# Optimization experiments

Hardware: AMD Instinct MI355X
Metric: run time of the kernel (lower is better)

## Reference

```python
import jax, jax.numpy as jnp
import numpy as np

SIZES = [384, 160, 128, 96, 1]   # aev_length followed by hidden sizes (ANI-1 config)
N_SPECIES = 4                    # H, C, N, O
N_LAYERS = 4
CELU_ALPHA = 0.1
B, A = 128, 512                  # molecules, atoms per molecule


def setup_inputs() -> dict:
    key = jax.random.key(0)
    ks = jax.random.split(key, 2 + 2 * N_LAYERS)
    inp = {
        "fullaev": jax.random.normal(ks[0], (B, A, SIZES[0]), dtype=jnp.float32),
        "species": jax.random.randint(ks[1], (A,), 0, N_SPECIES, dtype=jnp.int32),
    }
    # Per-species stacked Linear params, torch default init: U(-1/sqrt(fan_in), 1/sqrt(fan_in))
    for l in range(N_LAYERS):
        bound = 1.0 / np.sqrt(SIZES[l])
        inp[f"W{l}"] = jax.random.uniform(ks[2 + 2 * l], (N_SPECIES, SIZES[l + 1], SIZES[l]),
                                          dtype=jnp.float32, minval=-bound, maxval=bound)
        inp[f"b{l}"] = jax.random.uniform(ks[3 + 2 * l], (N_SPECIES, SIZES[l + 1]),
                                          dtype=jnp.float32, minval=-bound, maxval=bound)
    return inp


def reference(fullaev, species, W0, b0, W1, b1, W2, b2, W3, b3):
    # fullaev: [B, A, aev_len]; species: [A] int route ids.
    # Equivalent to the per-atom Python loop: each atom goes through its
    # species' MLP; gather the per-atom weight matrices and do one batched GEMM per layer.
    Ws = (W0, W1, W2, W3)
    bs = (b0, b1, b2, b3)
    y = fullaev
    for l in range(N_LAYERS):
        Wa = Ws[l][species]          # [A, out, in] gathered per atom
        ba = bs[l][species]          # [A, out]
        y = jnp.einsum('bai,aoi->bao', y, Wa) + ba[None, :, :]
        if l < N_LAYERS - 1:
            y = jax.nn.celu(y, alpha=CELU_ALPHA)
    # stack over atoms + sum reducer over atom dim, then squeeze -> [B]
    return jnp.squeeze(jnp.sum(y, axis=1), axis=-1)
```

## Files before the change

### kernel.cpp

```cpp
#include <hip/hip_runtime.h>


typedef float f32x4 __attribute__((ext_vector_type(4)));
typedef short s16x8 __attribute__((ext_vector_type(8)));

#define NMOL   128
#define NATOM  512
#define AEV    384
#define XLD    136
#define Y0LD   168
#define Y1LD   136
#define Y2LD   104

#define PL0    61440
#define PL1    20480
#define PL2    12288
#define BASE0  0
#define BASE1  245760
#define BASE2  327680
#define WP_BYTE_OFF 262144

__device__ __forceinline__ ushort f2bf(float f) {
    uint u = __float_as_uint(f);
    return (ushort)((u + 0x7fffu + ((u >> 16) & 1u)) >> 16);
}
__device__ __forceinline__ float bf2f(ushort h) {
    return __uint_as_float(((uint)h) << 16);
}
__device__ __forceinline__ float celu_f(float v) {
    return fmaxf(v, 0.0f) + fminf(0.1f * (__expf(10.0f * v) - 1.0f), 0.0f);
}

__global__ __launch_bounds__(256) void prep_kernel(
    const float* __restrict__ W0, const float* __restrict__ W1,
    const float* __restrict__ W2, ushort* __restrict__ Wp)
{
    const int idx = blockIdx.x * 256 + threadIdx.x;
    int n, k0, KS;
    size_t base;
    const float* src;
    if (idx < 30720) {
        const int s = idx / 7680, r = idx % 7680;
        n = r / 48; k0 = (r % 48) * 8; KS = 12;
        src = W0 + (size_t)idx * 8;
        base = BASE0 + (size_t)s * PL0;
    } else if (idx < 40960) {
        const int i2 = idx - 30720;
        const int s = i2 / 2560, r = i2 % 2560;
        n = r / 20; k0 = (r % 20) * 8; KS = 5;
        src = W1 + (size_t)i2 * 8;
        base = BASE1 + (size_t)s * PL1;
    } else {
        const int i2 = idx - 40960;
        const int s = i2 / 1536, r = i2 % 1536;
        n = r / 16; k0 = (r % 16) * 8; KS = 4;
        src = W2 + (size_t)i2 * 8;
        base = BASE2 + (size_t)s * PL2;
    }
    const float4 v0 = *(const float4*)(src);
    const float4 v1 = *(const float4*)(src + 4);
    const size_t fo = (size_t)((((n >> 4) * KS + (k0 >> 5)) * 64
                                + ((k0 & 31) >> 3) * 16 + (n & 15)) * 8);
    uint4 w;
    w.x = (uint)f2bf(v0.x) | ((uint)f2bf(v0.y) << 16);
    w.y = (uint)f2bf(v0.z) | ((uint)f2bf(v0.w) << 16);
    w.z = (uint)f2bf(v1.x) | ((uint)f2bf(v1.y) << 16);
    w.w = (uint)f2bf(v1.z) | ((uint)f2bf(v1.w) << 16);
    *(uint4*)(Wp + base + fo) = w;
}

__global__ __launch_bounds__(512, 4) void ani_mfma_kernel(
    const float* __restrict__ aev, const int* __restrict__ species,
    const ushort* __restrict__ Wp,
    const float* __restrict__ b0, const float* __restrict__ b1,
    const float* __restrict__ b2,
    const float* __restrict__ W3, const float* __restrict__ b3,
    float* __restrict__ partial)
{
    __shared__ __align__(16) ushort xbuf[NMOL * XLD];
    __shared__ __align__(16) ushort ybuf[NMOL * Y0LD];

    const int a    = blockIdx.x;
    const int tid  = threadIdx.x;
    const int lane = tid & 63;
    const int wid  = tid >> 6;
    const int mgrp = wid >> 2;
    const int ngrp = wid & 3;
    const bool has3 = (ngrp < 2);

    const int mol0 = tid >> 5;
    const int c4   = tid & 31;
    const size_t PSTR = (size_t)16 * NATOM * AEV;
    const float* xp = aev + ((size_t)mol0 * NATOM + a) * AEV + c4 * 4;

    const int s = species[a];
    const ushort* Bh0 = Wp + BASE0 + (size_t)s * PL0;
    const ushort* Bh1 = Wp + BASE1 + (size_t)s * PL1;
    const ushort* Bh2 = Wp + BASE2 + (size_t)s * PL2;
    const float* b0s = b0 + s * 160;
    const float* b1s = b1 + s * 128;
    const float* b2s = b2 + s * 96;
    const float* w3s = W3 + s * 96;
    const float  bb3 = b3[s];

    float4 rv[8];
    auto prefetch_rv = [&](int t) {
        #pragma unroll
        for (int p = 0; p < 8; ++p)
            rv[p] = *(const float4*)(xp + t * 128 + p * PSTR);
    };
    auto stage = [&]() {
        #pragma unroll
        for (int p = 0; p < 8; ++p) {
            uint2 ph;
            ph.x = (uint)f2bf(rv[p].x) | ((uint)f2bf(rv[p].y) << 16);
            ph.y = (uint)f2bf(rv[p].z) | ((uint)f2bf(rv[p].w) << 16);
            *(uint2*)(xbuf + (mol0 + 16 * p) * XLD + c4 * 4) = ph;
        }
    };

    f32x4 acc[4][3];
    const f32x4 zero = {0.f, 0.f, 0.f, 0.f};
    #pragma unroll
    for (int mf = 0; mf < 4; ++mf)
        #pragma unroll
        for (int t = 0; t < 3; ++t) acc[mf][t] = zero;

    prefetch_rv(0);
    stage();
    __syncthreads();

    #pragma unroll
    for (int tile = 0; tile < 3; ++tile) {
        if (tile < 2) prefetch_rv(tile + 1);
        #pragma unroll
        for (int ks = 0; ks < 4; ++ks) {
            const int gks = tile * 4 + ks;
            const s16x8 bh0 = *(const s16x8*)(Bh0 + ((size_t)((ngrp    ) * 12 + gks) * 64 + lane) * 8);
            const s16x8 bh1 = *(const s16x8*)(Bh0 + ((size_t)((ngrp + 4) * 12 + gks) * 64 + lane) * 8);
            s16x8 bh2;
            if (has3) bh2 = *(const s16x8*)(Bh0 + ((size_t)((ngrp + 8) * 12 + gks) * 64 + lane) * 8);
            s16x8 ah[4];
            #pragma unroll
            for (int mf = 0; mf < 4; ++mf)
                ah[mf] = *(const s16x8*)(xbuf + (mgrp * 64 + mf * 16 + (lane & 15)) * XLD
                                         + ks * 32 + (lane >> 4) * 8);
            #pragma unroll
            for (int mf = 0; mf < 4; ++mf) {
                acc[mf][0] = __builtin_amdgcn_mfma_f32_16x16x32_bf16(ah[mf], bh0, acc[mf][0], 0, 0, 0);
                acc[mf][1] = __builtin_amdgcn_mfma_f32_16x16x32_bf16(ah[mf], bh1, acc[mf][1], 0, 0, 0);
            }
            if (has3) {
                #pragma unroll
                for (int mf = 0; mf < 4; ++mf)
                    acc[mf][2] = __builtin_amdgcn_mfma_f32_16x16x32_bf16(ah[mf], bh2, acc[mf][2], 0, 0, 0);
            }
        }
        __syncthreads();
        if (tile < 2) {
            stage();
            __syncthreads();
        }
    }

    s16x8 b1r[2][5];
    #pragma unroll
    for (int ks = 0; ks < 5; ++ks) {
        b1r[0][ks] = *(const s16x8*)(Bh1 + ((size_t)((ngrp    ) * 5 + ks) * 64 + lane) * 8);
        b1r[1][ks] = *(const s16x8*)(Bh1 + ((size_t)((ngrp + 4) * 5 + ks) * 64 + lane) * 8);
    }

    #pragma unroll
    for (int t = 0; t < 3; ++t) {
        if (t < 2 || has3) {
            const int n = (ngrp + 4 * t) * 16 + (lane & 15);
            const float bv = b0s[n];
            #pragma unroll
            for (int mf = 0; mf < 4; ++mf) {
                #pragma unroll
                for (int r = 0; r < 4; ++r) {
                    const int row = mgrp * 64 + mf * 16 + (lane >> 4) * 4 + r;
                    ybuf[row * Y0LD + n] = f2bf(celu_f(acc[mf][t][r] + bv));
                }
            }
        }
    }
    __syncthreads();

    f32x4 acc1[4][2];
    #pragma unroll
    for (int mf = 0; mf < 4; ++mf) { acc1[mf][0] = zero; acc1[mf][1] = zero; }
    #pragma unroll
    for (int ks = 0; ks < 5; ++ks) {
        s16x8 ah[4];
        #pragma unroll
        for (int mf = 0; mf < 4; ++mf)
            ah[mf] = *(const s16x8*)(ybuf + (mgrp * 64 + mf * 16 + (lane & 15)) * Y0LD
                                     + ks * 32 + (lane >> 4) * 8);
        #pragma unroll
        for (int mf = 0; mf < 4; ++mf) {
            acc1[mf][0] = __builtin_amdgcn_mfma_f32_16x16x32_bf16(ah[mf], b1r[0][ks], acc1[mf][0], 0, 0, 0);
            acc1[mf][1] = __builtin_amdgcn_mfma_f32_16x16x32_bf16(ah[mf], b1r[1][ks], acc1[mf][1], 0, 0, 0);
        }
    }

    s16x8 b2r[2][4];
    #pragma unroll
    for (int ks = 0; ks < 4; ++ks)
        b2r[0][ks] = *(const s16x8*)(Bh2 + ((size_t)((ngrp) * 4 + ks) * 64 + lane) * 8);
    if (has3) {
        #pragma unroll
        for (int ks = 0; ks < 4; ++ks)
            b2r[1][ks] = *(const s16x8*)(Bh2 + ((size_t)((ngrp + 4) * 4 + ks) * 64 + lane) * 8);
    }

    #pragma unroll
    for (int t = 0; t < 2; ++t) {
        const int n = (ngrp + 4 * t) * 16 + (lane & 15);
        const float bv = b1s[n];
        #pragma unroll
        for (int mf = 0; mf < 4; ++mf) {
            #pragma unroll
            for (int r = 0; r < 4; ++r) {
                const int row = mgrp * 64 + mf * 16 + (lane >> 4) * 4 + r;
                xbuf[row * Y1LD + n] = f2bf(celu_f(acc1[mf][t][r] + bv));
            }
        }
    }
    __syncthreads();

    f32x4 acc2[4][2];
    #pragma unroll
    for (int mf = 0; mf < 4; ++mf) { acc2[mf][0] = zero; acc2[mf][1] = zero; }
    #pragma unroll
    for (int ks = 0; ks < 4; ++ks) {
        s16x8 ah[4];
        #pragma unroll
        for (int mf = 0; mf < 4; ++mf)
            ah[mf] = *(const s16x8*)(xbuf + (mgrp * 64 + mf * 16 + (lane & 15)) * Y1LD
                                     + ks * 32 + (lane >> 4) * 8);
        #pragma unroll
        for (int mf = 0; mf < 4; ++mf) {
            acc2[mf][0] = __builtin_amdgcn_mfma_f32_16x16x32_bf16(ah[mf], b2r[0][ks], acc2[mf][0], 0, 0, 0);
            if (has3)
                acc2[mf][1] = __builtin_amdgcn_mfma_f32_16x16x32_bf16(ah[mf], b2r[1][ks], acc2[mf][1], 0, 0, 0);
        }
    }
    __syncthreads();

    #pragma unroll
    for (int t = 0; t < 2; ++t) {
        if (t == 0 || has3) {
            const int n = (ngrp + 4 * t) * 16 + (lane & 15);
            const float bv = b2s[n];
            #pragma unroll
            for (int mf = 0; mf < 4; ++mf) {
                #pragma unroll
                for (int r = 0; r < 4; ++r) {
                    const int row = mgrp * 64 + mf * 16 + (lane >> 4) * 4 + r;
                    ybuf[row * Y2LD + n] = f2bf(celu_f(acc2[mf][t][r] + bv));
                }
            }
        }
    }
    __syncthreads();

    {
        float* red = (float*)xbuf;
        const int m = tid & (NMOL - 1);
        const int q = tid >> 7;
        float accv = 0.f;
        #pragma unroll
        for (int ii = 0; ii < 24; ++ii) {
            const int i = q * 24 + ii;
            accv = fmaf(w3s[i], bf2f(ybuf[m * Y2LD + i]), accv);
        }
        red[q * NMOL + m] = accv;
        __syncthreads();
        if (tid < NMOL) {
            const float sm = red[tid] + red[NMOL + tid] + red[2 * NMOL + tid]
                           + red[3 * NMOL + tid] + bb3;
            partial[(size_t)a * NMOL + tid] = sm;
        }
    }
}

__global__ __launch_bounds__(256) void reduce_kernel(
    const float* __restrict__ partial, float* __restrict__ out)
{
    __shared__ float red[256];
    const int m = blockIdx.x;
    const int t = threadIdx.x;
    float sv = partial[(size_t)t * NMOL + m] + partial[(size_t)(t + 256) * NMOL + m];
    red[t] = sv;
    __syncthreads();
    #pragma unroll
    for (int w = 128; w > 0; w >>= 1) {
        if (t < w) red[t] += red[t + w];
        __syncthreads();
    }
    if (t == 0) out[m] = red[0];
}

extern "C" void kernel_launch(void* const* d_in, const int* in_sizes, int n_in,
                              void* d_out, int out_size, void* d_ws, size_t ws_size,
                              hipStream_t stream) {
    const float* aev     = (const float*)d_in[0];
    const int*   species = (const int*)  d_in[1];
    const float* W0 = (const float*)d_in[2];
    const float* b0 = (const float*)d_in[3];
    const float* W1 = (const float*)d_in[4];
    const float* b1 = (const float*)d_in[5];
    const float* W2 = (const float*)d_in[6];
    const float* b2 = (const float*)d_in[7];
    const float* W3 = (const float*)d_in[8];
    const float* b3 = (const float*)d_in[9];
    float* out     = (float*)d_out;
    float* partial = (float*)d_ws;
    ushort* Wp     = (ushort*)((char*)d_ws + WP_BYTE_OFF);

    prep_kernel<<<184, 256, 0, stream>>>(W0, W1, W2, Wp);
    ani_mfma_kernel<<<NATOM, 512, 0, stream>>>(aev, species, Wp,
                                               b0, b1, b2, W3, b3, partial);
    reduce_kernel<<<NMOL, 256, 0, stream>>>(partial, out);
}
```

Baseline: 44.57 us.

## Double-buffer layer-0 input staging in LDS with smaller K tiles

Splits the layer-0 input staging into six K=64 tiles held in two LDS buffers, with a two-slot register prefetch that runs two tiles ahead. Each tile now needs one barrier instead of two, so the next tile can be staged while the current one is being multiplied. This trades fewer MFMA steps per barrier and slightly more LDS for less barrier stall on the global loads. The launch-bounds attribute is restated in explicit amdgpu attribute form.

```diff
diff --git a/kernel.cpp b/kernel.cpp
--- a/kernel.cpp
+++ b/kernel.cpp
@@ -7,7 +7,7 @@
 #define NMOL   128
 #define NATOM  512
 #define AEV    384
-#define XLD    136
+#define XLD    72
 #define Y0LD   168
 #define Y1LD   136
 #define Y2LD   104
@@ -69,7 +69,9 @@
     *(uint4*)(Wp + base + fo) = w;
 }
 
-__global__ __launch_bounds__(512, 4) void ani_mfma_kernel(
+__global__ __attribute__((amdgpu_flat_work_group_size(512, 512),
+                          amdgpu_waves_per_eu(4, 4)))
+void ani_mfma_kernel(
     const float* __restrict__ aev, const int* __restrict__ species,
     const ushort* __restrict__ Wp,
     const float* __restrict__ b0, const float* __restrict__ b1,
@@ -77,7 +79,7 @@
     const float* __restrict__ W3, const float* __restrict__ b3,
     float* __restrict__ partial)
 {
-    __shared__ __align__(16) ushort xbuf[NMOL * XLD];
+    __shared__ __align__(16) ushort xbuf[2 * NMOL * XLD];
     __shared__ __align__(16) ushort ybuf[NMOL * Y0LD];
 
     const int a    = blockIdx.x;
@@ -88,9 +90,9 @@
     const int ngrp = wid & 3;
     const bool has3 = (ngrp < 2);
 
-    const int mol0 = tid >> 5;
-    const int c4   = tid & 31;
-    const size_t PSTR = (size_t)16 * NATOM * AEV;
+    const int mol0 = tid >> 4;
+    const int c4   = tid & 15;
+    const size_t PSTR = (size_t)32 * NATOM * AEV;
     const float* xp = aev + ((size_t)mol0 * NATOM + a) * AEV + c4 * 4;
 
     const int s = species[a];
@@ -103,19 +105,22 @@
     const float* w3s = W3 + s * 96;
     const float  bb3 = b3[s];
 
-    float4 rv[8];
-    auto prefetch_rv = [&](int t) {
-        #pragma unroll
-        for (int p = 0; p < 8; ++p)
-            rv[p] = *(const float4*)(xp + t * 128 + p * PSTR);
+    ushort* X0 = xbuf;
+    ushort* X1 = xbuf + NMOL * XLD;
+
+    float4 rv[2][4];
+    auto prefetch_rv = [&](int slot, int t) {
+        #pragma unroll
+        for (int p = 0; p < 4; ++p)
+            rv[slot][p] = *(const float4*)(xp + t * 64 + p * PSTR);
     };
-    auto stage = [&]() {
-        #pragma unroll
-        for (int p = 0; p < 8; ++p) {
+    auto stage = [&](ushort* dst, int slot) {
+        #pragma unroll
+        for (int p = 0; p < 4; ++p) {
             uint2 ph;
-            ph.x = (uint)f2bf(rv[p].x) | ((uint)f2bf(rv[p].y) << 16);
-            ph.y = (uint)f2bf(rv[p].z) | ((uint)f2bf(rv[p].w) << 16);
-            *(uint2*)(xbuf + (mol0 + 16 * p) * XLD + c4 * 4) = ph;
+            ph.x = (uint)f2bf(rv[slot][p].x) | ((uint)f2bf(rv[slot][p].y) << 16);
+            ph.y = (uint)f2bf(rv[slot][p].z) | ((uint)f2bf(rv[slot][p].w) << 16);
+            *(uint2*)(dst + (mol0 + 32 * p) * XLD + c4 * 4) = ph;
         }
     };
 
@@ -126,16 +131,20 @@
         #pragma unroll
         for (int t = 0; t < 3; ++t) acc[mf][t] = zero;
 
-    prefetch_rv(0);
-    stage();
-    __syncthreads();
-
-    #pragma unroll
-    for (int tile = 0; tile < 3; ++tile) {
-        if (tile < 2) prefetch_rv(tile + 1);
-        #pragma unroll
-        for (int ks = 0; ks < 4; ++ks) {
-            const int gks = tile * 4 + ks;
+    prefetch_rv(0, 0);
+    stage(X0, 0);
+    prefetch_rv(1, 1);
+    __syncthreads();
+
+    #pragma unroll
+    for (int t = 0; t < 6; ++t) {
+        const int cur = t & 1;
+        ushort* Xc = cur ? X1 : X0;
+        ushort* Xn = cur ? X0 : X1;
+        if (t < 4) prefetch_rv(cur, t + 2);
+        #pragma unroll
+        for (int ks = 0; ks < 2; ++ks) {
+            const int gks = t * 2 + ks;
             const s16x8 bh0 = *(const s16x8*)(Bh0 + ((size_t)((ngrp    ) * 12 + gks) * 64 + lane) * 8);
             const s16x8 bh1 = *(const s16x8*)(Bh0 + ((size_t)((ngrp + 4) * 12 + gks) * 64 + lane) * 8);
             s16x8 bh2;
@@ -143,7 +152,7 @@
             s16x8 ah[4];
             #pragma unroll
             for (int mf = 0; mf < 4; ++mf)
-                ah[mf] = *(const s16x8*)(xbuf + (mgrp * 64 + mf * 16 + (lane & 15)) * XLD
+                ah[mf] = *(const s16x8*)(Xc + (mgrp * 64 + mf * 16 + (lane & 15)) * XLD
                                          + ks * 32 + (lane >> 4) * 8);
             #pragma unroll
             for (int mf = 0; mf < 4; ++mf) {
@@ -156,9 +165,8 @@
                     acc[mf][2] = __builtin_amdgcn_mfma_f32_16x16x32_bf16(ah[mf], bh2, acc[mf][2], 0, 0, 0);
             }
         }
-        __syncthreads();
-        if (tile < 2) {
-            stage();
+        if (t < 5) {
+            stage(Xn, cur ^ 1);
             __syncthreads();
         }
     }
```

Result: faster. 42.97 us (-3.6%).

## Load layer-0 A fragments directly from global, drop LDS staging of AEV

Applied to the files above, without the earlier changes.

Layer 0 no longer stages the AEV tile through shared memory with syncs between K tiles. Each wave now loads its MFMA A-fragments straight from global memory, converts them to bf16 in registers, and works on a different wave tiling (4 M-groups by 2 N-groups, 5 N-fragments each). This is meant to remove the LDS round trip and barriers from the dominant GEMM. In exchange the global loads are strided per lane, there is no explicit prefetch, and register pressure rises with 10 accumulators. The launch-bounds attribute is also switched to explicit waves-per-eu.

```diff
diff --git a/kernel.cpp b/kernel.cpp
--- a/kernel.cpp
+++ b/kernel.cpp
@@ -1,4 +1,5 @@
 #include <hip/hip_runtime.h>
+#include <hip/hip_bf16.h>
 
 
 typedef float f32x4 __attribute__((ext_vector_type(4)));
@@ -7,7 +8,6 @@
 #define NMOL   128
 #define NATOM  512
 #define AEV    384
-#define XLD    136
 #define Y0LD   168
 #define Y1LD   136
 #define Y2LD   104
@@ -29,6 +29,12 @@
 }
 __device__ __forceinline__ float celu_f(float v) {
     return fmaxf(v, 0.0f) + fminf(0.1f * (__expf(10.0f * v) - 1.0f), 0.0f);
+}
+__device__ __forceinline__ uint pk2bf(float x, float y) {
+    __hip_bfloat162 h2;
+    h2.x = __float2bfloat16(x);
+    h2.y = __float2bfloat16(y);
+    return *(uint*)&h2;
 }
 
 __global__ __launch_bounds__(256) void prep_kernel(
@@ -69,7 +75,9 @@
     *(uint4*)(Wp + base + fo) = w;
 }
 
-__global__ __launch_bounds__(512, 4) void ani_mfma_kernel(
+__global__ __attribute__((amdgpu_flat_work_group_size(512, 512),
+                          amdgpu_waves_per_eu(4, 4)))
+void ani_mfma_kernel(
     const float* __restrict__ aev, const int* __restrict__ species,
     const ushort* __restrict__ Wp,
     const float* __restrict__ b0, const float* __restrict__ b1,
@@ -77,21 +85,13 @@
     const float* __restrict__ W3, const float* __restrict__ b3,
     float* __restrict__ partial)
 {
-    __shared__ __align__(16) ushort xbuf[NMOL * XLD];
-    __shared__ __align__(16) ushort ybuf[NMOL * Y0LD];
+    __shared__ __align__(16) ushort y0buf[NMOL * Y0LD];
+    __shared__ __align__(16) ushort y1buf[NMOL * Y1LD];
 
     const int a    = blockIdx.x;
     const int tid  = threadIdx.x;
     const int lane = tid & 63;
     const int wid  = tid >> 6;
-    const int mgrp = wid >> 2;
-    const int ngrp = wid & 3;
-    const bool has3 = (ngrp < 2);
-
-    const int mol0 = tid >> 5;
-    const int c4   = tid & 31;
-    const size_t PSTR = (size_t)16 * NATOM * AEV;
-    const float* xp = aev + ((size_t)mol0 * NATOM + a) * AEV + c4 * 4;
 
     const int s = species[a];
     const ushort* Bh0 = Wp + BASE0 + (size_t)s * PL0;
@@ -103,177 +103,158 @@
     const float* w3s = W3 + s * 96;
     const float  bb3 = b3[s];
 
-    float4 rv[8];
-    auto prefetch_rv = [&](int t) {
-        #pragma unroll
-        for (int p = 0; p < 8; ++p)
-            rv[p] = *(const float4*)(xp + t * 128 + p * PSTR);
-    };
-    auto stage = [&]() {
-        #pragma unroll
-        for (int p = 0; p < 8; ++p) {
-            uint2 ph;
-            ph.x = (uint)f2bf(rv[p].x) | ((uint)f2bf(rv[p].y) << 16);
-            ph.y = (uint)f2bf(rv[p].z) | ((uint)f2bf(rv[p].w) << 16);
-            *(uint2*)(xbuf + (mol0 + 16 * p) * XLD + c4 * 4) = ph;
-        }
-    };
-
-    f32x4 acc[4][3];
     const f32x4 zero = {0.f, 0.f, 0.f, 0.f};
-    #pragma unroll
-    for (int mf = 0; mf < 4; ++mf)
-        #pragma unroll
-        for (int t = 0; t < 3; ++t) acc[mf][t] = zero;
-
-    prefetch_rv(0);
-    stage();
-    __syncthreads();
-
-    #pragma unroll
-    for (int tile = 0; tile < 3; ++tile) {
-        if (tile < 2) prefetch_rv(tile + 1);
-        #pragma unroll
-        for (int ks = 0; ks < 4; ++ks) {
-            const int gks = tile * 4 + ks;
-            const s16x8 bh0 = *(const s16x8*)(Bh0 + ((size_t)((ngrp    ) * 12 + gks) * 64 + lane) * 8);
-            const s16x8 bh1 = *(const s16x8*)(Bh0 + ((size_t)((ngrp + 4) * 12 + gks) * 64 + lane) * 8);
-            s16x8 bh2;
-            if (has3) bh2 = *(const s16x8*)(Bh0 + ((size_t)((ngrp + 8) * 12 + gks) * 64 + lane) * 8);
-            s16x8 ah[4];
-            #pragma unroll
-            for (int mf = 0; mf < 4; ++mf)
-                ah[mf] = *(const s16x8*)(xbuf + (mgrp * 64 + mf * 16 + (lane & 15)) * XLD
-                                         + ks * 32 + (lane >> 4) * 8);
-            #pragma unroll
-            for (int mf = 0; mf < 4; ++mf) {
-                acc[mf][0] = __builtin_amdgcn_mfma_f32_16x16x32_bf16(ah[mf], bh0, acc[mf][0], 0, 0, 0);
-                acc[mf][1] = __builtin_amdgcn_mfma_f32_16x16x32_bf16(ah[mf], bh1, acc[mf][1], 0, 0, 0);
-            }
-            if (has3) {
+
+    {
+        const int mgrp0 = wid >> 1;
+        const int ngrp0 = wid & 1;
+        const float* arow = aev + ((size_t)(mgrp0 * 32 + (lane & 15)) * NATOM + a) * AEV
+                            + (lane >> 4) * 8;
+        const size_t AMF = (size_t)16 * NATOM * AEV;
+
+        f32x4 acc0[2][5];
+        #pragma unroll
+        for (int mf = 0; mf < 2; ++mf)
+            #pragma unroll
+            for (int nf = 0; nf < 5; ++nf) acc0[mf][nf] = zero;
+
+        #pragma unroll
+        for (int gks = 0; gks < 12; ++gks) {
+            s16x8 ah[2];
+            #pragma unroll
+            for (int mf = 0; mf < 2; ++mf) {
+                const float* ap = arow + mf * AMF + gks * 32;
+                const float4 lo = *(const float4*)(ap);
+                const float4 hi = *(const float4*)(ap + 4);
+                union { s16x8 v; uint u[4]; } r;
+                r.u[0] = pk2bf(lo.x, lo.y);
+                r.u[1] = pk2bf(lo.z, lo.w);
+                r.u[2] = pk2bf(hi.x, hi.y);
+                r.u[3] = pk2bf(hi.z, hi.w);
+                ah[mf] = r.v;
+            }
+            #pragma unroll
+            for (int nf = 0; nf < 5; ++nf) {
+                const s16x8 bh = *(const s16x8*)(
+                    Bh0 + ((size_t)((ngrp0 * 5 + nf) * 12 + gks) * 64 + lane) * 8);
+                acc0[0][nf] = __builtin_amdgcn_mfma_f32_16x16x32_bf16(ah[0], bh, acc0[0][nf], 0, 0, 0);
+                acc0[1][nf] = __builtin_amdgcn_mfma_f32_16x16x32_bf16(ah[1], bh, acc0[1][nf], 0, 0, 0);
+            }
+        }
+
+        #pragma unroll
+        for (int nf = 0; nf < 5; ++nf) {
+            const int n = (ngrp0 * 5 + nf) * 16 + (lane & 15);
+            const float bv = b0s[n];
+            #pragma unroll
+            for (int mf = 0; mf < 2; ++mf) {
                 #pragma unroll
-                for (int mf = 0; mf < 4; ++mf)
-                    acc[mf][2] = __builtin_amdgcn_mfma_f32_16x16x32_bf16(ah[mf], bh2, acc[mf][2], 0, 0, 0);
-            }
-        }
-        __syncthreads();
-        if (tile < 2) {
-            stage();
-            __syncthreads();
-        }
-    }
-
+                for (int r = 0; r < 4; ++r) {
+                    const int row = mgrp0 * 32 + mf * 16 + (lane >> 4) * 4 + r;
+                    y0buf[row * Y0LD + n] = f2bf(celu_f(acc0[mf][nf][r] + bv));
+                }
+            }
+        }
+    }
+
+    const int mgrp = wid >> 2;
+    const int ngrp = wid & 3;
+    const bool has3 = (ngrp < 2);
     s16x8 b1r[2][5];
     #pragma unroll
     for (int ks = 0; ks < 5; ++ks) {
         b1r[0][ks] = *(const s16x8*)(Bh1 + ((size_t)((ngrp    ) * 5 + ks) * 64 + lane) * 8);
         b1r[1][ks] = *(const s16x8*)(Bh1 + ((size_t)((ngrp + 4) * 5 + ks) * 64 + lane) * 8);
     }
-
-    #pragma unroll
-    for (int t = 0; t < 3; ++t) {
-        if (t < 2 || has3) {
+    __syncthreads();
+
+    f32x4 acc1[4][2];
+    #pragma unroll
+    for (int mf = 0; mf < 4; ++mf) { acc1[mf][0] = zero; acc1[mf][1] = zero; }
+    #pragma unroll
+    for (int ks = 0; ks < 5; ++ks) {
+        s16x8 ah[4];
+        #pragma unroll
+        for (int mf = 0; mf < 4; ++mf)
+            ah[mf] = *(const s16x8*)(y0buf + (mgrp * 64 + mf * 16 + (lane & 15)) * Y0LD
+                                     + ks * 32 + (lane >> 4) * 8);
+        #pragma unroll
+        for (int mf = 0; mf < 4; ++mf) {
+            acc1[mf][0] = __builtin_amdgcn_mfma_f32_16x16x32_bf16(ah[mf], b1r[0][ks], acc1[mf][0], 0, 0, 0);
+            acc1[mf][1] = __builtin_amdgcn_mfma_f32_16x16x32_bf16(ah[mf], b1r[1][ks], acc1[mf][1], 0, 0, 0);
+        }
+    }
+
+    s16x8 b2r[2][4];
+    #pragma unroll
+    for (int ks = 0; ks < 4; ++ks)
+        b2r[0][ks] = *(const s16x8*)(Bh2 + ((size_t)((ngrp) * 4 + ks) * 64 + lane) * 8);
+    if (has3) {
+        #pragma unroll
+        for (int ks = 0; ks < 4; ++ks)
+            b2r[1][ks] = *(const s16x8*)(Bh2 + ((size_t)((ngrp + 4) * 4 + ks) * 64 + lane) * 8);
+    }
+
+    #pragma unroll
+    for (int t = 0; t < 2; ++t) {
+        const int n = (ngrp + 4 * t) * 16 + (lane & 15);
+        const float bv = b1s[n];
+        #pragma unroll
+        for (int mf = 0; mf < 4; ++mf) {
+            #pragma unroll
+            for (int r = 0; r < 4; ++r) {
+                const int row = mgrp * 64 + mf * 16 + (lane >> 4) * 4 + r;
+                y1buf[row * Y1LD + n] = f2bf(celu_f(acc1[mf][t][r] + bv));
+            }
+        }
+    }
+    __syncthreads();
+
+    f32x4 acc2[4][2];
+    #pragma unroll
+    for (int mf = 0; mf < 4; ++mf) { acc2[mf][0] = zero; acc2[mf][1] = zero; }
+    #pragma unroll
+    for (int ks = 0; ks < 4; ++ks) {
+        s16x8 ah[4];
+        #pragma unroll
+        for (int mf = 0; mf < 4; ++mf)
+            ah[mf] = *(const s16x8*)(y1buf + (mgrp * 64 + mf * 16 + (lane & 15)) * Y1LD
+                                     + ks * 32 + (lane >> 4) * 8);
+        #pragma unroll
+        for (int mf = 0; mf < 4; ++mf) {
+            acc2[mf][0] = __builtin_amdgcn_mfma_f32_16x16x32_bf16(ah[mf], b2r[0][ks], acc2[mf][0], 0, 0, 0);
+            if (has3)
+                acc2[mf][1] = __builtin_amdgcn_mfma_f32_16x16x32_bf16(ah[mf], b2r[1][ks], acc2[mf][1], 0, 0, 0);
+        }
+    }
+    __syncthreads();
+
+    #pragma unroll
+    for (int t = 0; t < 2; ++t) {
+        if (t == 0 || has3) {
             const int n = (ngrp + 4 * t) * 16 + (lane & 15);
-            const float bv = b0s[n];
+            const float bv = b2s[n];
             #pragma unroll
             for (int mf = 0; mf < 4; ++mf) {
                 #pragma unroll
                 for (int r = 0; r < 4; ++r) {
                     const int row = mgrp * 64 + mf * 16 + (lane >> 4) * 4 + r;
-                    ybuf[row * Y0LD + n] = f2bf(celu_f(acc[mf][t][r] + bv));
+                    y0buf[row * Y2LD + n] = f2bf(celu_f(acc2[mf][t][r] + bv));
                 }
             }
         }
     }
     __syncthreads();
 
-    f32x4 acc1[4][2];
-    #pragma unroll
-    for (int mf = 0; mf < 4; ++mf) { acc1[mf][0] = zero; acc1[mf][1] = zero; }
-    #pragma unroll
-    for (int ks = 0; ks < 5; ++ks) {
-        s16x8 ah[4];
-        #pragma unroll
-        for (int mf = 0; mf < 4; ++mf)
-            ah[mf] = *(const s16x8*)(ybuf + (mgrp * 64 + mf * 16 + (lane & 15)) * Y0LD
-                                     + ks * 32 + (lane >> 4) * 8);
-        #pragma unroll
-        for (int mf = 0; mf < 4; ++mf) {
-            acc1[mf][0] = __builtin_amdgcn_mfma_f32_16x16x32_bf16(ah[mf], b1r[0][ks], acc1[mf][0], 0, 0, 0);
-            acc1[mf][1] = __builtin_amdgcn_mfma_f32_16x16x32_bf16(ah[mf], b1r[1][ks], acc1[mf][1], 0, 0, 0);
-        }
-    }
-
-    s16x8 b2r[2][4];
-    #pragma unroll
-    for (int ks = 0; ks < 4; ++ks)
-        b2r[0][ks] = *(const s16x8*)(Bh2 + ((size_t)((ngrp) * 4 + ks) * 64 + lane) * 8);
-    if (has3) {
-        #pragma unroll
-        for (int ks = 0; ks < 4; ++ks)
-            b2r[1][ks] = *(const s16x8*)(Bh2 + ((size_t)((ngrp + 4) * 4 + ks) * 64 + lane) * 8);
-    }
-
-    #pragma unroll
-    for (int t = 0; t < 2; ++t) {
-        const int n = (ngrp + 4 * t) * 16 + (lane & 15);
-        const float bv = b1s[n];
-        #pragma unroll
-        for (int mf = 0; mf < 4; ++mf) {
-            #pragma unroll
-            for (int r = 0; r < 4; ++r) {
-                const int row = mgrp * 64 + mf * 16 + (lane >> 4) * 4 + r;
-                xbuf[row * Y1LD + n] = f2bf(celu_f(acc1[mf][t][r] + bv));
-            }
-        }
-    }
-    __syncthreads();
-
-    f32x4 acc2[4][2];
-    #pragma unroll
-    for (int mf = 0; mf < 4; ++mf) { acc2[mf][0] = zero; acc2[mf][1] = zero; }
-    #pragma unroll
-    for (int ks = 0; ks < 4; ++ks) {
-        s16x8 ah[4];
-        #pragma unroll
-        for (int mf = 0; mf < 4; ++mf)
-            ah[mf] = *(const s16x8*)(xbuf + (mgrp * 64 + mf * 16 + (lane & 15)) * Y1LD
-                                     + ks * 32 + (lane >> 4) * 8);
-        #pragma unroll
-        for (int mf = 0; mf < 4; ++mf) {
-            acc2[mf][0] = __builtin_amdgcn_mfma_f32_16x16x32_bf16(ah[mf], b2r[0][ks], acc2[mf][0], 0, 0, 0);
-            if (has3)
-                acc2[mf][1] = __builtin_amdgcn_mfma_f32_16x16x32_bf16(ah[mf], b2r[1][ks], acc2[mf][1], 0, 0, 0);
-        }
-    }
-    __syncthreads();
-
-    #pragma unroll
-    for (int t = 0; t < 2; ++t) {
-        if (t == 0 || has3) {
-            const int n = (ngrp + 4 * t) * 16 + (lane & 15);
-            const float bv = b2s[n];
-            #pragma unroll
-            for (int mf = 0; mf < 4; ++mf) {
-                #pragma unroll
-                for (int r = 0; r < 4; ++r) {
-                    const int row = mgrp * 64 + mf * 16 + (lane >> 4) * 4 + r;
-                    ybuf[row * Y2LD + n] = f2bf(celu_f(acc2[mf][t][r] + bv));
-                }
-            }
-        }
-    }
-    __syncthreads();
-
     {
-        float* red = (float*)xbuf;
+        float* red = (float*)y1buf;
         const int m = tid & (NMOL - 1);
         const int q = tid >> 7;
         float accv = 0.f;
         #pragma unroll
         for (int ii = 0; ii < 24; ++ii) {
             const int i = q * 24 + ii;
-            accv = fmaf(w3s[i], bf2f(ybuf[m * Y2LD + i]), accv);
+            accv = fmaf(w3s[i], bf2f(y0buf[m * Y2LD + i]), accv);
         }
         red[q * NMOL + m] = accv;
         __syncthreads();
```

Result: slower. 52.22 us (+17.2%).
